# Performance work log

Hardware: AMD Instinct MI355X
Metric: run time of the kernel (lower is better)

Reference implementation:

```python
import math
import jax, jax.numpy as jnp
import numpy as np

NHEAD = 16
HEAD_DIM = 64
D_MODEL = 1024
B, T = 2, 4096


def setup_inputs() -> dict:
    key = jax.random.key(0)
    ks = jax.random.split(key, 9)
    HD = NHEAD * HEAD_DIM
    s_in = 1.0 / math.sqrt(D_MODEL)
    s_out = 1.0 / math.sqrt(HD)
    return {
        "x": jax.random.normal(ks[0], (B, T, D_MODEL), dtype=jnp.float32),
        "Wq": jax.random.normal(ks[1], (D_MODEL, HD), dtype=jnp.float32) * s_in,
        "bq": jnp.zeros((HD,), dtype=jnp.float32),
        "Wk": jax.random.normal(ks[2], (D_MODEL, HD), dtype=jnp.float32) * s_in,
        "bk": jnp.zeros((HD,), dtype=jnp.float32),
        "Wv": jax.random.normal(ks[3], (D_MODEL, HD), dtype=jnp.float32) * s_in,
        "bv": jnp.zeros((HD,), dtype=jnp.float32),
        "Wo": jax.random.normal(ks[4], (HD, D_MODEL), dtype=jnp.float32) * s_out,
        "bo": jnp.zeros((D_MODEL,), dtype=jnp.float32),
    }


def _cosformer(x, Wq, bq, Wk, bk, Wv, bv, Wo, bo):
    Bsz, Tlen, _ = x.shape
    H, dh = NHEAD, HEAD_DIM
    # projections -> [B, T, H, dh]
    Q = (x @ Wq + bq).reshape(Bsz, Tlen, H, dh)
    K = (x @ Wk + bk).reshape(Bsz, Tlen, H, dh)
    V = (x @ Wv + bv).reshape(Bsz, Tlen, H, dh)
    Qp = jax.nn.relu(Q)
    Kp = jax.nn.relu(K)
    # cosFormer position reweighting: angle_i = pi/(2M) * i, M = T
    angles = (math.pi / (2.0 * Tlen)) * jnp.arange(Tlen, dtype=jnp.float32)
    cosw = jnp.cos(angles)[None, :, None, None]
    sinw = jnp.sin(angles)[None, :, None, None]
    Qc, Qs = Qp * cosw, Qp * sinw
    Kc, Ks = Kp * cosw, Kp * sinw
    # scan over time with O(d^2) causal state instead of materializing (B,H,T,d,d)
    # reorder to time-major [T, B, H, dh]
    tm = lambda a: jnp.moveaxis(a, 1, 0)
    Qc, Qs, Kc, Ks, Vt = tm(Qc), tm(Qs), tm(Kc), tm(Ks), tm(V)

    S0 = jnp.zeros((Bsz, H, dh, dh), dtype=x.dtype)
    z0 = jnp.zeros((Bsz, H, dh), dtype=x.dtype)

    def step(carry, inp):
        S_cos, S_sin, z_cos, z_sin = carry
        qc, qs, kc, ks_, v = inp  # each [B, H, dh]
        S_cos = S_cos + kc[..., :, None] * v[..., None, :]
        S_sin = S_sin + ks_[..., :, None] * v[..., None, :]
        z_cos = z_cos + kc
        z_sin = z_sin + ks_
        num = jnp.einsum('bhi,bhij->bhj', qc, S_cos) + jnp.einsum('bhi,bhij->bhj', qs, S_sin)
        den = jnp.sum(qc * z_cos + qs * z_sin, axis=-1)
        den = jnp.maximum(den, 1e-6)[..., None]
        return (S_cos, S_sin, z_cos, z_sin), num / den

    _, out = jax.lax.scan(step, (S0, S0, z0, z0), (Qc, Qs, Kc, Ks, Vt))
    # out: [T, B, H, dh] -> [B, T, H*dh]
    out = jnp.moveaxis(out, 0, 1).reshape(Bsz, Tlen, H * dh)
    return out @ Wo + bo


def reference(x, Wq, bq, Wk, bk, Wv, bv, Wo, bo):
    return _cosformer(x, Wq, bq, Wk, bk, Wv, bv, Wo, bo)
```

## Files before the change

### kernel.cpp

```cpp
#include <hip/hip_runtime.h>

#define NTOK   8192
#define DM     1024
#define HD_    1024
#define TSEQ   4096
#define NCH    64
#define SROWS  72
#define SHALF  (SROWS*64)
#define SSTR   (2*SHALF)
#define ANG_STEP 3.8349519697141029e-4f

typedef _Float16 h8_t  __attribute__((ext_vector_type(8)));
typedef _Float16 h4_t  __attribute__((ext_vector_type(4)));
typedef float    f32x4 __attribute__((ext_vector_type(4)));

__device__ __forceinline__ void gload16(const void* g, void* l) {
    __builtin_amdgcn_global_load_lds(
        (const __attribute__((address_space(1))) void*)g,
        (__attribute__((address_space(3))) void*)l, 16, 0, 0);
}

__device__ __forceinline__ void gemm_core(
    const _Float16* __restrict__ A, const _Float16* __restrict__ Wt,
    const float* __restrict__ bias, int mode,
    _Float16* rows16, _Float16* tp16, float* rows32, char* sm)
{
    const int tid = threadIdx.x;
    const int lane = tid & 63, w = tid >> 6;
    const int m_base = blockIdx.x * 128, n_base = blockIdx.y * 128;

    const int r0 = tid >> 2;
    const int cb0 = (tid & 3) << 4;
    const _Float16* ga = A  + (size_t)(m_base + r0) * DM + (cb0 >> 1);
    const _Float16* gb = Wt + (size_t)(n_base + r0) * DM + (cb0 >> 1);
    char* lA = sm + w * 1024;
    char* lB = sm + 8192 + w * 1024;
    char* Ct = sm;

    f32x4 acc[4][4];
#pragma unroll
    for (int i = 0; i < 4; ++i)
#pragma unroll
        for (int j = 0; j < 4; ++j) acc[i][j] = (f32x4){0.f, 0.f, 0.f, 0.f};

    const int wm = (w >> 1) * 64, wn = (w & 1) * 64;
    const int fr = lane & 15;
    const int fk = (lane >> 4) * 16;

    for (int kt = 0; kt < DM / 32; ++kt) {
        const int k0 = kt * 32;
        __syncthreads();
        gload16(ga + k0,           lA);
        gload16(ga + 64 * DM + k0, lA + 4096);
        gload16(gb + k0,           lB);
        gload16(gb + 64 * DM + k0, lB + 4096);
        __syncthreads();
        h8_t a[4], b[4];
#pragma unroll
        for (int i = 0; i < 4; ++i) {
            a[i] = *(const h8_t*)(sm + (wm + i * 16 + fr) * 64 + fk);
            b[i] = *(const h8_t*)(sm + 8192 + (wn + i * 16 + fr) * 64 + fk);
        }
#pragma unroll
        for (int i = 0; i < 4; ++i)
#pragma unroll
            for (int j = 0; j < 4; ++j)
                acc[i][j] = __builtin_amdgcn_mfma_f32_16x16x32_f16(a[i], b[j], acc[i][j], 0, 0, 0);
    }

    const int rm = (lane >> 4) * 4;
    if (mode == 3) {
#pragma unroll
        for (int j = 0; j < 4; ++j) {
            const int col = n_base + wn + j * 16 + fr;
            const float bs = bias[col];
#pragma unroll
            for (int i = 0; i < 4; ++i) {
                const int m0 = m_base + wm + i * 16 + rm;
#pragma unroll
                for (int r = 0; r < 4; ++r)
                    rows32[(size_t)(m0 + r) * HD_ + col] = acc[i][j][r] + bs;
            }
        }
        return;
    }

    __syncthreads();

    if (mode <= 1) {
#pragma unroll
        for (int j = 0; j < 4; ++j) {
            const int col = wn + j * 16 + fr;
            const float bs = bias[n_base + col];
#pragma unroll
            for (int i = 0; i < 4; ++i) {
                const int ml0 = wm + i * 16 + rm;
#pragma unroll
                for (int r = 0; r < 4; ++r) {
                    const int mloc = ml0 + r;
                    const int byte = ((mloc << 8) + (col << 1)) ^ ((mloc & 15) << 4);
                    *(_Float16*)(Ct + byte) = (_Float16)fmaxf(acc[i][j][r] + bs, 0.f);
                }
            }
        }
        __syncthreads();
#pragma unroll
        for (int p = 0; p < 8; ++p) {
            const int lin = p * 256 + tid;
            const int t = lin >> 4, d8 = lin & 15;
            h8_t v = *(const h8_t*)(Ct + (t << 8) + ((d8 ^ (t & 15)) << 4));
            *(h8_t*)(rows16 + (size_t)(m_base + t) * HD_ + n_base + d8 * 8) = v;
        }
    }

    if (mode >= 1) {
        if (mode == 1) __syncthreads();
#pragma unroll
        for (int j = 0; j < 4; ++j) {
            const int col = wn + j * 16 + fr;
            const float bs = bias[n_base + col];
#pragma unroll
            for (int i = 0; i < 4; ++i) {
                const int ml0 = wm + i * 16 + rm;
                h4_t pk;
#pragma unroll
                for (int r = 0; r < 4; ++r) {
                    float v = acc[i][j][r] + bs;
                    if (mode == 1) v = fmaxf(v, 0.f);
                    pk[r] = (_Float16)v;
                }
                const int byte = ((col << 8) + (ml0 << 1)) ^ ((col & 15) << 4);
                *(h4_t*)(Ct + byte) = pk;
            }
        }
        __syncthreads();
        const int bb = m_base >> 12;
        const int tl0 = m_base & 4095;
#pragma unroll
        for (int p = 0; p < 8; ++p) {
            const int lin = p * 256 + tid;
            const int d = lin >> 4, t8 = lin & 15;
            h8_t v = *(const h8_t*)(Ct + (d << 8) + ((t8 ^ (d & 15)) << 4));
            const int colg = n_base + d;
            *(h8_t*)(tp16 + ((size_t)(bb * 16 + (colg >> 6)) * 64 + (colg & 63)) * TSEQ
                     + tl0 + t8 * 8) = v;
        }
    }
}

__global__ __launch_bounds__(256) void gemm_qkv(
    const _Float16* __restrict__ Xh, const _Float16* __restrict__ WtQKV,
    const float* __restrict__ bq, const float* __restrict__ bk, const float* __restrict__ bv,
    _Float16* __restrict__ Qh, _Float16* __restrict__ Kh,
    _Float16* __restrict__ KT, _Float16* __restrict__ VT)
{
    __shared__ char sm[32768];
    const int z = blockIdx.z;
    const _Float16* Wt = WtQKV + (size_t)z * (DM * HD_);
    const float* bias = (z == 0) ? bq : (z == 1) ? bk : bv;
    _Float16* r16 = (z == 0) ? Qh : Kh;
    _Float16* t16 = (z == 1) ? KT : VT;
    gemm_core(Xh, Wt, bias, z, r16, t16, nullptr, sm);
}

__global__ __launch_bounds__(256) void gemm_out(
    const _Float16* __restrict__ A, const _Float16* __restrict__ Wt,
    const float* __restrict__ bias, float* __restrict__ out)
{
    __shared__ char sm[16384];
    gemm_core(A, Wt, bias, 3, nullptr, nullptr, out, sm);
}

__global__ __launch_bounds__(256) void conv_x_kernel(
    const float* __restrict__ x, _Float16* __restrict__ xh)
{
    const int i = blockIdx.x * 256 + threadIdx.x;
    float4 v = ((const float4*)x)[i];
    h4_t hv;
    hv[0] = (_Float16)v.x; hv[1] = (_Float16)v.y;
    hv[2] = (_Float16)v.z; hv[3] = (_Float16)v.w;
    ((h4_t*)xh)[i] = hv;
}

__global__ __launch_bounds__(256) void conv_wt4(
    const float* __restrict__ Wq, const float* __restrict__ Wk,
    const float* __restrict__ Wv, const float* __restrict__ Wo,
    _Float16* __restrict__ WtQKV, _Float16* __restrict__ WtO)
{
    __shared__ float t[32][33];
    const int z = blockIdx.z;
    const float* W = (z == 0) ? Wq : (z == 1) ? Wk : (z == 2) ? Wv : Wo;
    _Float16* Wt = (z < 3) ? WtQKV + (size_t)z * DM * HD_ : WtO;
    const int bx = blockIdx.x * 32, by = blockIdx.y * 32;
    const int tx = threadIdx.x, ty = threadIdx.y;
#pragma unroll
    for (int i = 0; i < 4; ++i)
        t[ty + 8 * i][tx] = W[(size_t)(by + ty + 8 * i) * HD_ + bx + tx];
    __syncthreads();
#pragma unroll
    for (int i = 0; i < 4; ++i)
        Wt[(size_t)(bx + ty + 8 * i) * DM + by + tx] = (_Float16)t[tx][ty + 8 * i];
}

__global__ __launch_bounds__(256) void chunk_sums(
    const _Float16* __restrict__ KT, const _Float16* __restrict__ VT,
    _Float16* __restrict__ states)
{
    __shared__ char sm[26880];
    _Float16* cwh = (_Float16*)(sm);
    _Float16* swh = (_Float16*)(sm + 128);
    #define CS_KC 256
    #define CS_KS 8448
    #define CS_VT 16640

    const int c = blockIdx.x, bh = blockIdx.y;
    const int tid = threadIdx.x, lane = tid & 63, w = tid >> 6;

    if (tid < 64) {
        float s_, c_;
        sincosf(ANG_STEP * (float)(c * 64 + tid), &s_, &c_);
        cwh[tid] = (_Float16)c_; swh[tid] = (_Float16)s_;
    }
    __syncthreads();

    const size_t ktb = (size_t)(bh * 64) * TSEQ + c * 64;
#pragma unroll
    for (int rnd = 0; rnd < 2; ++rnd) {
        int lin = rnd * 256 + tid;
        int r = lin >> 3, u = lin & 7;
        h8_t kv = *(const h8_t*)(KT + ktb + (size_t)r * TSEQ + u * 8);
        h8_t c8 = *(const h8_t*)&cwh[u * 8];
        h8_t s8 = *(const h8_t*)&swh[u * 8];
        int sb = (r * 128 + u * 16) ^ ((r & 7) << 4);
        *(h8_t*)(sm + CS_KC + sb) = kv * c8;
        *(h8_t*)(sm + CS_KS + sb) = kv * s8;
    }
    const _Float16* vtb = VT + (size_t)(bh * 64) * TSEQ + c * 64;
#pragma unroll
    for (int rnd = 0; rnd < 2; ++rnd) {
        int lin = rnd * 256 + tid;
        int r = lin >> 3, u = lin & 7;
        gload16(vtb + (size_t)r * TSEQ + (u ^ (r & 7)) * 8,
                sm + CS_VT + (rnd * 256 + w * 64) * 16);
    }
    if (tid < 8) {
        h8_t one;
#pragma unroll
        for (int e = 0; e < 8; ++e) one[e] = (_Float16)1.0f;
        *(h8_t*)(sm + CS_VT + 64 * 128 + tid * 16) = one;
    }
    __syncthreads();

    const int fr = lane & 15, rm = (lane >> 4) * 4;
    _Float16* stc = states + (size_t)(bh * NCH + c) * SSTR;

    for (int half = 0; half < 2; ++half) {
        const int ko = half ? CS_KS : CS_KC;
        f32x4 acc[4][5];
#pragma unroll
        for (int i = 0; i < 4; ++i)
#pragma unroll
            for (int j = 0; j < 5; ++j) acc[i][j] = (f32x4){0.f, 0.f, 0.f, 0.f};
#pragma unroll
        for (int ks = 0; ks < 2; ++ks) {
            const int fko = ks * 64 + (lane >> 4) * 16;
            h8_t af[4], bf[5];
#pragma unroll
            for (int i = 0; i < 4; ++i) {
                int row = i * 16 + fr;
                af[i] = *(const h8_t*)(sm + ko + ((row * 128 + fko) ^ ((row & 7) << 4)));
            }
#pragma unroll
            for (int j = 0; j < 5; ++j) {
                int row = j * 16 + fr;
                bf[j] = *(const h8_t*)(sm + CS_VT + ((row * 128 + fko) ^ ((row & 7) << 4)));
            }
#pragma unroll
            for (int i = 0; i < 4; ++i)
#pragma unroll
                for (int j = 0; j < 5; ++j)
                    acc[i][j] = __builtin_amdgcn_mfma_f32_16x16x32_f16(af[i], bf[j], acc[i][j], 0, 0, 0);
        }
        _Float16* dst = stc + half * SHALF;
#pragma unroll
        for (int j = 0; j < 5; ++j) {
            int n = j * 16 + fr;
#pragma unroll
            for (int i = 0; i < 4; ++i) {
                h4_t pk;
#pragma unroll
                for (int r = 0; r < 4; ++r) pk[r] = (_Float16)acc[i][j][r];
                if (n <= 64) *(h4_t*)(dst + (size_t)n * 64 + i * 16 + rm) = pk;
            }
        }
    }
}

__global__ __launch_bounds__(256) void scan_kernel(_Float16* __restrict__ states)
{
    const int e8 = blockIdx.x * 256 + threadIdx.x;
    if (e8 >= SSTR / 8) return;
    _Float16* p = states + (size_t)blockIdx.y * (NCH * (size_t)SSTR) + (size_t)e8 * 8;
    float run[8];
#pragma unroll
    for (int e = 0; e < 8; ++e) run[e] = 0.f;
    for (int c = 0; c < NCH; ++c) {
        h8_t v = *(const h8_t*)(p + (size_t)c * SSTR);
        h8_t ov;
#pragma unroll
        for (int e = 0; e < 8; ++e) {
            ov[e] = (_Float16)run[e];
            run[e] += (float)v[e];
        }
        *(h8_t*)(p + (size_t)c * SSTR) = ov;
    }
}

__global__ __launch_bounds__(256) void attn_mfma(
    const _Float16* __restrict__ Qh, const _Float16* __restrict__ Kh,
    const _Float16* __restrict__ VT, const _Float16* __restrict__ states,
    _Float16* __restrict__ atth)
{
    __shared__ char sm[53248];
    float* cwf = (float*)(sm);
    float* swf = (float*)(sm + 256);
    _Float16* cwh = (_Float16*)(sm + 512);
    _Float16* swh = (_Float16*)(sm + 640);
    #define AT_Q 768
    #define AT_K 8960
    #define AT_A 17152
    #define AT_V 25344
    #define AT_C 33792
    #define AT_S 43008

    const int c = blockIdx.x, bh = blockIdx.y;
    const int b = bh >> 4, h = bh & 15;
    const int tid = threadIdx.x, lane = tid & 63, w = tid >> 6;
    const int tok0 = b * TSEQ + c * 64;

    if (tid < 64) {
        float s_, c_;
        sincosf(ANG_STEP * (float)(c * 64 + tid), &s_, &c_);
        cwf[tid] = c_; swf[tid] = s_;
        cwh[tid] = (_Float16)c_; swh[tid] = (_Float16)s_;
    }

    const _Float16* stb = states + (size_t)(bh * NCH + c) * SSTR;
#pragma unroll
    for (int rnd = 0; rnd < 2; ++rnd) {
        int lin = rnd * 256 + tid;
        int r = lin >> 3, u = lin & 7;
        int su = (u ^ (r & 7)) * 8;
        char* lb = sm + (rnd * 256 + w * 64) * 16;
        gload16(Qh + (size_t)(tok0 + r) * HD_ + h * 64 + su, lb + AT_Q);
        gload16(Kh + (size_t)(tok0 + r) * HD_ + h * 64 + su, lb + AT_K);
        gload16(VT + (size_t)(bh * 64 + r) * TSEQ + c * 64 + su, lb + AT_V);
    }
#pragma unroll
    for (int rnd = 0; rnd < 3; ++rnd) {
        if (rnd < 2 || tid < 64) {
            int lin = rnd * 256 + tid;
            int r = lin >> 3, u = lin & 7;
            int su = (u ^ (r & 7)) * 8;
            char* lb = sm + (rnd * 256 + w * 64) * 16;
            gload16(stb + (size_t)r * 64 + su, lb + AT_C);
            gload16(stb + SHALF + (size_t)r * 64 + su, lb + AT_S);
        }
    }
    if (tid < 8) {
        h8_t one;
#pragma unroll
        for (int e = 0; e < 8; ++e) one[e] = (_Float16)1.0f;
        *(h8_t*)(sm + AT_V + 64 * 128 + tid * 16) = one;
    }
    __syncthreads();

    const int fr = lane & 15;
    f32x4 dt[4][4];
#pragma unroll
    for (int i = 0; i < 4; ++i)
#pragma unroll
        for (int j = 0; j < 4; ++j) dt[i][j] = (f32x4){0.f, 0.f, 0.f, 0.f};
#pragma unroll
    for (int ks = 0; ks < 2; ++ks) {
        const int fko = ks * 64 + (lane >> 4) * 16;
        h8_t ak[4], bq[4];
#pragma unroll
        for (int i = 0; i < 4; ++i) {
            int row = i * 16 + fr;
            int sb = (row * 128 + fko) ^ ((row & 7) << 4);
            ak[i] = *(const h8_t*)(sm + AT_K + sb);
            bq[i] = *(const h8_t*)(sm + AT_Q + sb);
        }
#pragma unroll
        for (int i = 0; i < 4; ++i)
#pragma unroll
            for (int j = 0; j < 4; ++j)
                dt[i][j] = __builtin_amdgcn_mfma_f32_16x16x32_f16(ak[i], bq[j], dt[i][j], 0, 0, 0);
    }
    {
        const int sr0 = (lane >> 4) * 4;
#pragma unroll
        for (int j = 0; j < 4; ++j) {
            const int tt = j * 16 + fr;
            const float cwt = cwf[tt], swt = swf[tt];
#pragma unroll
            for (int i = 0; i < 4; ++i) {
                const int s0 = i * 16 + sr0;
                h4_t pk;
#pragma unroll
                for (int r = 0; r < 4; ++r) {
                    int s = s0 + r;
                    float f = cwt * cwf[s] + swt * swf[s];
                    float a = (s <= tt) ? dt[i][j][r] * f : 0.f;
                    pk[r] = (_Float16)a;
                }
                int sb = (tt * 128 + s0 * 2) ^ ((tt & 7) << 4);
                *(h4_t*)(sm + AT_A + sb) = pk;
            }
        }
    }
    __syncthreads();

    f32x4 o[4][5];
#pragma unroll
    for (int i = 0; i < 4; ++i)
#pragma unroll
        for (int j = 0; j < 5; ++j) o[i][j] = (f32x4){0.f, 0.f, 0.f, 0.f};
#pragma unroll
    for (int ks = 0; ks < 2; ++ks) {
        const int fko = ks * 64 + (lane >> 4) * 16;
        h8_t aa[4], aqc[4], aqs[4];
#pragma unroll
        for (int i = 0; i < 4; ++i) {
            int row = i * 16 + fr;
            int sb = (row * 128 + fko) ^ ((row & 7) << 4);
            aa[i] = *(const h8_t*)(sm + AT_A + sb);
            h8_t q8 = *(const h8_t*)(sm + AT_Q + sb);
            aqc[i] = q8 * cwh[row];
            aqs[i] = q8 * swh[row];
        }
#pragma unroll
        for (int j = 0; j < 5; ++j) {
            int row = j * 16 + fr;
            int sb = (row * 128 + fko) ^ ((row & 7) << 4);
            h8_t bv = *(const h8_t*)(sm + AT_V + sb);
            h8_t bc = *(const h8_t*)(sm + AT_C + sb);
            h8_t bs = *(const h8_t*)(sm + AT_S + sb);
#pragma unroll
            for (int i = 0; i < 4; ++i) {
                o[i][j] = __builtin_amdgcn_mfma_f32_16x16x32_f16(aa[i],  bv, o[i][j], 0, 0, 0);
                o[i][j] = __builtin_amdgcn_mfma_f32_16x16x32_f16(aqc[i], bc, o[i][j], 0, 0, 0);
                o[i][j] = __builtin_amdgcn_mfma_f32_16x16x32_f16(aqs[i], bs, o[i][j], 0, 0, 0);
            }
        }
    }
    char* Ce = sm + AT_K;
    const int rm = (lane >> 4) * 4;
#pragma unroll
    for (int i = 0; i < 4; ++i) {
        float rden[4];
#pragma unroll
        for (int r = 0; r < 4; ++r)
            rden[r] = 1.0f / fmaxf(__shfl(o[i][4][r], lane & 48), 1e-6f);
#pragma unroll
        for (int j = 0; j < 4; ++j) {
            const int col = j * 16 + fr;
#pragma unroll
            for (int r = 0; r < 4; ++r) {
                const int t = i * 16 + rm + r;
                const int byte = ((t << 7) + (col << 1)) ^ ((t & 7) << 4);
                *(_Float16*)(Ce + byte) = (_Float16)(o[i][j][r] * rden[r]);
            }
        }
    }
    __syncthreads();
#pragma unroll
    for (int p = 0; p < 2; ++p) {
        const int lin = p * 256 + tid;
        const int t = lin >> 3, d8 = lin & 7;
        h8_t v = *(const h8_t*)(Ce + (t << 7) + ((d8 ^ (t & 7)) << 4));
        *(h8_t*)(atth + (size_t)(tok0 + t) * HD_ + h * 64 + d8 * 8) = v;
    }
}

extern "C" void kernel_launch(void* const* d_in, const int* in_sizes, int n_in,
                              void* d_out, int out_size, void* d_ws, size_t ws_size,
                              hipStream_t stream)
{
    const float* x  = (const float*)d_in[0];
    const float* Wq = (const float*)d_in[1];
    const float* bq = (const float*)d_in[2];
    const float* Wk = (const float*)d_in[3];
    const float* bk = (const float*)d_in[4];
    const float* Wv = (const float*)d_in[5];
    const float* bv = (const float*)d_in[6];
    const float* Wo = (const float*)d_in[7];
    const float* bo = (const float*)d_in[8];
    float* out = (float*)d_out;

    _Float16* ws = (_Float16*)d_ws;
    _Float16* Xh     = ws;
    _Float16* WtQKV  = Xh + (size_t)NTOK * DM;
    _Float16* WtO    = WtQKV + 3 * (size_t)DM * HD_;
    _Float16* Qh     = WtO + (size_t)DM * HD_;
    _Float16* Kh     = Qh + (size_t)NTOK * HD_;
    _Float16* KT     = Kh + (size_t)NTOK * HD_;
    _Float16* VT     = KT + (size_t)NTOK * HD_;
    _Float16* atth   = VT + (size_t)NTOK * HD_;
    _Float16* states = atth + (size_t)NTOK * HD_;

    dim3 tb(256);
    hipLaunchKernelGGL(conv_x_kernel, dim3(NTOK * DM / 1024), tb, 0, stream, x, Xh);
    hipLaunchKernelGGL(conv_wt4, dim3(32, 32, 4), dim3(32, 8), 0, stream,
                       Wq, Wk, Wv, Wo, WtQKV, WtO);
    hipLaunchKernelGGL(gemm_qkv, dim3(64, 8, 3), tb, 0, stream,
                       Xh, WtQKV, bq, bk, bv, Qh, Kh, KT, VT);
    hipLaunchKernelGGL(chunk_sums, dim3(NCH, 32), tb, 0, stream, KT, VT, states);
    hipLaunchKernelGGL(scan_kernel, dim3(5, 32), tb, 0, stream, states);
    hipLaunchKernelGGL(attn_mfma, dim3(NCH, 32), tb, 0, stream, Qh, Kh, VT, states, atth);
    hipLaunchKernelGGL(gemm_out, dim3(64, 8), tb, 0, stream, atth, WtO, bo, out);
}
```

Baseline: 299.2 us.

## Halve QKV GEMM LDS via two-pass epilogue, interleave Q/K/V tiles, unroll scan

The QKV GEMM epilogue now stages the output tile through shared memory in two 64-row or 64-column halves instead of one full 128x128 tile. This cuts the kernel's shared allocation from 32KB to 16KB, which should allow more resident blocks per CU. The grid is flattened so that Q, K and V tiles for the same row block are adjacent in launch order, which may improve L2 reuse of X. The chunk-state scan loop is also unrolled by four to batch its loads and stores, at the cost of extra barriers in the epilogue.

New measurement: 305.9 us. 1.02x slower.

```diff
diff --git a/kernel.cpp b/kernel.cpp
--- a/kernel.cpp
+++ b/kernel.cpp
@@ -22,12 +22,11 @@
 
 __device__ __forceinline__ void gemm_core(
     const _Float16* __restrict__ A, const _Float16* __restrict__ Wt,
-    const float* __restrict__ bias, int mode,
+    const float* __restrict__ bias, int mode, int m_base, int n_base,
     _Float16* rows16, _Float16* tp16, float* rows32, char* sm)
 {
     const int tid = threadIdx.x;
     const int lane = tid & 63, w = tid >> 6;
-    const int m_base = blockIdx.x * 128, n_base = blockIdx.y * 128;
 
     const int r0 = tid >> 2;
     const int cb0 = (tid & 3) << 4;
@@ -88,62 +87,74 @@
     __syncthreads();
 
     if (mode <= 1) {
-#pragma unroll
-        for (int j = 0; j < 4; ++j) {
-            const int col = wn + j * 16 + fr;
-            const float bs = bias[n_base + col];
-#pragma unroll
-            for (int i = 0; i < 4; ++i) {
-                const int ml0 = wm + i * 16 + rm;
-#pragma unroll
-                for (int r = 0; r < 4; ++r) {
-                    const int mloc = ml0 + r;
-                    const int byte = ((mloc << 8) + (col << 1)) ^ ((mloc & 15) << 4);
-                    *(_Float16*)(Ct + byte) = (_Float16)fmaxf(acc[i][j][r] + bs, 0.f);
+        const int myhalf = w >> 1;
+#pragma unroll
+        for (int pass = 0; pass < 2; ++pass) {
+            if (myhalf == pass) {
+#pragma unroll
+                for (int j = 0; j < 4; ++j) {
+                    const int col = wn + j * 16 + fr;
+                    const float bs = bias[n_base + col];
+#pragma unroll
+                    for (int i = 0; i < 4; ++i) {
+#pragma unroll
+                        for (int r = 0; r < 4; ++r) {
+                            const int t = i * 16 + rm + r;
+                            const int byte = ((t << 8) + (col << 1)) ^ ((t & 15) << 4);
+                            *(_Float16*)(Ct + byte) = (_Float16)fmaxf(acc[i][j][r] + bs, 0.f);
+                        }
+                    }
                 }
             }
-        }
-        __syncthreads();
-#pragma unroll
-        for (int p = 0; p < 8; ++p) {
-            const int lin = p * 256 + tid;
-            const int t = lin >> 4, d8 = lin & 15;
-            h8_t v = *(const h8_t*)(Ct + (t << 8) + ((d8 ^ (t & 15)) << 4));
-            *(h8_t*)(rows16 + (size_t)(m_base + t) * HD_ + n_base + d8 * 8) = v;
+            __syncthreads();
+#pragma unroll
+            for (int p = 0; p < 4; ++p) {
+                const int lin = p * 256 + tid;
+                const int t = lin >> 4, d8 = lin & 15;
+                h8_t v = *(const h8_t*)(Ct + (t << 8) + ((d8 ^ (t & 15)) << 4));
+                *(h8_t*)(rows16 + (size_t)(m_base + pass * 64 + t) * HD_ + n_base + d8 * 8) = v;
+            }
+            __syncthreads();
         }
     }
 
     if (mode >= 1) {
-        if (mode == 1) __syncthreads();
-#pragma unroll
-        for (int j = 0; j < 4; ++j) {
-            const int col = wn + j * 16 + fr;
-            const float bs = bias[n_base + col];
-#pragma unroll
-            for (int i = 0; i < 4; ++i) {
-                const int ml0 = wm + i * 16 + rm;
-                h4_t pk;
-#pragma unroll
-                for (int r = 0; r < 4; ++r) {
-                    float v = acc[i][j][r] + bs;
-                    if (mode == 1) v = fmaxf(v, 0.f);
-                    pk[r] = (_Float16)v;
-                }
-                const int byte = ((col << 8) + (ml0 << 1)) ^ ((col & 15) << 4);
-                *(h4_t*)(Ct + byte) = pk;
-            }
-        }
-        __syncthreads();
+        const int myside = w & 1;
         const int bb = m_base >> 12;
         const int tl0 = m_base & 4095;
 #pragma unroll
-        for (int p = 0; p < 8; ++p) {
-            const int lin = p * 256 + tid;
-            const int d = lin >> 4, t8 = lin & 15;
-            h8_t v = *(const h8_t*)(Ct + (d << 8) + ((t8 ^ (d & 15)) << 4));
-            const int colg = n_base + d;
-            *(h8_t*)(tp16 + ((size_t)(bb * 16 + (colg >> 6)) * 64 + (colg & 63)) * TSEQ
-                     + tl0 + t8 * 8) = v;
+        for (int pass = 0; pass < 2; ++pass) {
+            if (myside == pass) {
+#pragma unroll
+                for (int j = 0; j < 4; ++j) {
+                    const int coll = j * 16 + fr;
+                    const float bs = bias[n_base + pass * 64 + coll];
+#pragma unroll
+                    for (int i = 0; i < 4; ++i) {
+                        const int ml0 = wm + i * 16 + rm;
+                        h4_t pk;
+#pragma unroll
+                        for (int r = 0; r < 4; ++r) {
+                            float v = acc[i][j][r] + bs;
+                            if (mode == 1) v = fmaxf(v, 0.f);
+                            pk[r] = (_Float16)v;
+                        }
+                        const int byte = ((coll << 8) + (ml0 << 1)) ^ ((coll & 15) << 4);
+                        *(h4_t*)(Ct + byte) = pk;
+                    }
+                }
+            }
+            __syncthreads();
+#pragma unroll
+            for (int p = 0; p < 4; ++p) {
+                const int lin = p * 256 + tid;
+                const int d = lin >> 4, t8 = lin & 15;
+                h8_t v = *(const h8_t*)(Ct + (d << 8) + ((t8 ^ (d & 15)) << 4));
+                const int colg = n_base + pass * 64 + d;
+                *(h8_t*)(tp16 + ((size_t)(bb * 16 + (colg >> 6)) * 64 + (colg & 63)) * TSEQ
+                         + tl0 + t8 * 8) = v;
+            }
+            __syncthreads();
         }
     }
 }
@@ -154,13 +165,14 @@
     _Float16* __restrict__ Qh, _Float16* __restrict__ Kh,
     _Float16* __restrict__ KT, _Float16* __restrict__ VT)
 {
-    __shared__ char sm[32768];
-    const int z = blockIdx.z;
+    __shared__ char sm[16384];
+    const int bx = blockIdx.x;
+    const int z = bx % 3, mtile = bx / 3;
     const _Float16* Wt = WtQKV + (size_t)z * (DM * HD_);
     const float* bias = (z == 0) ? bq : (z == 1) ? bk : bv;
     _Float16* r16 = (z == 0) ? Qh : Kh;
     _Float16* t16 = (z == 1) ? KT : VT;
-    gemm_core(Xh, Wt, bias, z, r16, t16, nullptr, sm);
+    gemm_core(Xh, Wt, bias, z, mtile * 128, blockIdx.y * 128, r16, t16, nullptr, sm);
 }
 
 __global__ __launch_bounds__(256) void gemm_out(
@@ -168,7 +180,8 @@
     const float* __restrict__ bias, float* __restrict__ out)
 {
     __shared__ char sm[16384];
-    gemm_core(A, Wt, bias, 3, nullptr, nullptr, out, sm);
+    gemm_core(A, Wt, bias, 3, blockIdx.x * 128, blockIdx.y * 128,
+              nullptr, nullptr, out, sm);
 }
 
 __global__ __launch_bounds__(256) void conv_x_kernel(
@@ -304,15 +317,23 @@
     float run[8];
 #pragma unroll
     for (int e = 0; e < 8; ++e) run[e] = 0.f;
-    for (int c = 0; c < NCH; ++c) {
-        h8_t v = *(const h8_t*)(p + (size_t)c * SSTR);
-        h8_t ov;
+    for (int c = 0; c < NCH; c += 4) {
+        h8_t v0 = *(const h8_t*)(p + (size_t)(c + 0) * SSTR);
+        h8_t v1 = *(const h8_t*)(p + (size_t)(c + 1) * SSTR);
+        h8_t v2 = *(const h8_t*)(p + (size_t)(c + 2) * SSTR);
+        h8_t v3 = *(const h8_t*)(p + (size_t)(c + 3) * SSTR);
+        h8_t o0, o1, o2, o3;
 #pragma unroll
         for (int e = 0; e < 8; ++e) {
-            ov[e] = (_Float16)run[e];
-            run[e] += (float)v[e];
-        }
-        *(h8_t*)(p + (size_t)c * SSTR) = ov;
+            o0[e] = (_Float16)run[e]; run[e] += (float)v0[e];
+            o1[e] = (_Float16)run[e]; run[e] += (float)v1[e];
+            o2[e] = (_Float16)run[e]; run[e] += (float)v2[e];
+            o3[e] = (_Float16)run[e]; run[e] += (float)v3[e];
+        }
+        *(h8_t*)(p + (size_t)(c + 0) * SSTR) = o0;
+        *(h8_t*)(p + (size_t)(c + 1) * SSTR) = o1;
+        *(h8_t*)(p + (size_t)(c + 2) * SSTR) = o2;
+        *(h8_t*)(p + (size_t)(c + 3) * SSTR) = o3;
     }
 }
 
@@ -514,7 +535,7 @@
     hipLaunchKernelGGL(conv_x_kernel, dim3(NTOK * DM / 1024), tb, 0, stream, x, Xh);
     hipLaunchKernelGGL(conv_wt4, dim3(32, 32, 4), dim3(32, 8), 0, stream,
                        Wq, Wk, Wv, Wo, WtQKV, WtO);
-    hipLaunchKernelGGL(gemm_qkv, dim3(64, 8, 3), tb, 0, stream,
+    hipLaunchKernelGGL(gemm_qkv, dim3(192, 8), tb, 0, stream,
                        Xh, WtQKV, bq, bk, bv, Qh, Kh, KT, VT);
     hipLaunchKernelGGL(chunk_sums, dim3(NCH, 32), tb, 0, stream, KT, VT, states);
     hipLaunchKernelGGL(scan_kernel, dim3(5, 32), tb, 0, stream, states);
```
